# Optimization experiments

Hardware: AMD Instinct MI355X
Metric: run time of the kernel (lower is better)

## Reference

```python
import jax, jax.numpy as jnp
import numpy as np

B_, L, DM = 4, 1024, 1024
DI, DS, DR, DC = 1024, 16, 64, 4
NH = 4
DK = DM // NH


def setup_inputs() -> dict:
    key = jax.random.key(0)
    ks = jax.random.split(key, 16)
    def w(i, shape, scale=0.02):
        return jax.random.normal(ks[i], shape, dtype=jnp.float32) * scale
    inp = {
        "x": jax.random.normal(ks[0], (B_, L, DM), dtype=jnp.float32),
        "xx": jax.random.normal(ks[1], (B_, L, DI), dtype=jnp.float32),
        "in_proj_w": w(2, (DI, DM)),
        "conv_w": w(3, (DI, 1, DC)),            # depthwise conv, groups=DI
        "conv_b": jnp.zeros((DI,), jnp.float32),
        "x_proj_w": w(4, (DR + 2 * DS, DI)),
        "dt_proj_w": w(5, (DI, DR)),
        "dt_proj_b": jnp.zeros((DI,), jnp.float32),
        "A_log": jnp.log(jnp.tile(jnp.arange(1, DS + 1, dtype=jnp.float32)[None, :], (DI, 1))),
        "D": jnp.ones((DI,), jnp.float32),
        "wq": w(6, (DM, DM)), "bq": jnp.zeros((DM,), jnp.float32),
        "wk": w(7, (DM, DM)), "bk": jnp.zeros((DM,), jnp.float32),
        "wv": w(8, (DM, DM)), "bv": jnp.zeros((DM,), jnp.float32),
        "wo": w(9, (DM, DM)), "bo": jnp.zeros((DM,), jnp.float32),
    }
    return inp


def _stim_forward(x, xx, in_proj_w, conv_w, conv_b, x_proj_w, dt_proj_w, dt_proj_b,
                  A_log, D, wq, bq, wk, bk, wv, bv, wo, bo):
    b, l, _ = xx.shape
    # query branch: in_proj (Linear, no bias)
    q = x @ in_proj_w.T                                    # (b, l, DI)
    # kv branch: causal depthwise conv1d (padding d_conv-1, truncated to l)
    xc = jnp.transpose(xx, (0, 2, 1))                      # (b, DI, l)
    xc = jax.lax.conv_general_dilated(
        xc, conv_w, window_strides=(1,), padding=[(DC - 1, 0)],
        dimension_numbers=("NCH", "OIH", "NCH"), feature_group_count=DI)
    xc = xc + conv_b[None, :, None]
    u = jax.nn.silu(jnp.transpose(xc, (0, 2, 1)))          # (b, l, DI)
    # SSM parameter projections
    A = -jnp.exp(A_log)                                    # (DI, DS)
    x_dbl = u @ x_proj_w.T                                 # (b, l, DR+2*DS)
    delta, Bm, Cm = jnp.split(x_dbl, [DR, DR + DS], axis=-1)
    delta = jax.nn.softplus(delta @ dt_proj_w.T + dt_proj_b)  # (b, l, DI)
    deltaA = jnp.exp(jnp.einsum("bld,dn->bldn", delta, A))    # (b, l, DI, DS)
    deltaBu = jnp.einsum("bld,bln,bld->bldn", delta, Bm, u)   # (b, l, DI, DS)
    # selective scan over time
    def step(h, inp):
        dA_t, dBu_t, C_t = inp
        h = dA_t * h + dBu_t                               # (b, DI, DS)
        y_t = jnp.einsum("bdn,bn->bd", h, C_t)             # (b, DI)
        return h, y_t
    h0 = jnp.zeros((b, DI, DS), dtype=u.dtype)
    _, ys = jax.lax.scan(step, h0, (jnp.moveaxis(deltaA, 1, 0),
                                    jnp.moveaxis(deltaBu, 1, 0),
                                    jnp.moveaxis(Cm, 1, 0)))
    y = jnp.moveaxis(ys, 0, 1) + u * D                     # (b, l, DI)
    # cross attention: query = q, key/value = y
    Q = (q @ wq.T + bq).reshape(b, l, NH, DK).transpose(0, 2, 1, 3)
    K = (y @ wk.T + bk).reshape(b, l, NH, DK).transpose(0, 2, 1, 3)
    V = (y @ wv.T + bv).reshape(b, l, NH, DK).transpose(0, 2, 1, 3)
    scale = 1.0 / np.sqrt(DK).astype(np.float32)
    scores = jnp.einsum("bhqd,bhkd->bhqk", Q, K) * scale
    attn = jax.nn.softmax(scores, axis=-1)
    out = jnp.einsum("bhqk,bhkd->bhqd", attn, V)
    out = out.transpose(0, 2, 1, 3).reshape(b, l, DM)
    return out @ wo.T + bo


def reference(x, xx, in_proj_w, conv_w, conv_b, x_proj_w, dt_proj_w, dt_proj_b,
              A_log, D, wq, bq, wk, bk, wv, bv, wo, bo):
    return _stim_forward(x, xx, in_proj_w, conv_w, conv_b, x_proj_w, dt_proj_w,
                         dt_proj_b, A_log, D, wq, bq, wk, bk, wv, bv, wo, bo)
```

## Files before the change

### kernel.cpp

```cpp
#include <hip/hip_runtime.h>
#include <math.h>

#define B_  4
#define L_  1024
#define DM  1024
#define DI  1024
#define DS  16
#define DR  64
#define DCV 4
#define NH  4
#define DK  256

#define NCH 32
#define CHL (L_ / NCH)

typedef __attribute__((ext_vector_type(8))) short short8;
typedef __attribute__((ext_vector_type(4))) float floatx4;

static __device__ __forceinline__ unsigned short f2bf(float f) {
    unsigned int u = __float_as_uint(f);
    u += 0x7fffu + ((u >> 16) & 1u);
    return (unsigned short)(u >> 16);
}
static __device__ __forceinline__ float bf2f(unsigned short s) {
    return __uint_as_float(((unsigned int)s) << 16);
}

#define GLL(gp, lp) __builtin_amdgcn_global_load_lds( \
        (const __attribute__((address_space(1))) void*)(gp), \
        (__attribute__((address_space(3))) void*)(lp), 16, 0, 0)

static __device__ __forceinline__ void xcd_rect(int gx, int gy, int& tx, int& ty)
{
    int n = blockIdx.x + gx * blockIdx.y;
    if ((gx & 1) == 0 && (gy & 3) == 0) {
        int xcd = n & 7, j = n >> 3;
        int hx = gx >> 1, qy = gy >> 2;
        tx = (xcd & 1) * hx + (j % hx);
        ty = (xcd >> 1) * qy + (j / hx);
    } else {
        tx = blockIdx.x; ty = blockIdx.y;
    }
}

struct PrepArgs {
    const float* xx; const float* cw; const float* cb;
    float* u; unsigned short* ub;
    const float* xs; unsigned short* xd;
    const float* s[7]; unsigned short* d[7];
    int n[7];
    int ns[7];
};

__global__ __launch_bounds__(256) void prep(PrepArgs pa)
{
    int bid = blockIdx.x, tid = threadIdx.x;
    if (bid < 16384) {
        int idx = bid * 256 + tid;
        int d = idx & (DI - 1);
        int l = (idx >> 10) & (L_ - 1);
        int b = idx >> 20;
        const float* xb = pa.xx + (size_t)b * L_ * DI + d;
        float z = pa.cb[d];
#pragma unroll
        for (int j = 0; j < DCV; j++) {
            int t = l - (DCV - 1) + j;
            if (t >= 0) z += xb[(size_t)t * DI] * pa.cw[d * DCV + j];
        }
        float v = z / (1.0f + __expf(-z));
        pa.u[idx] = v;
        pa.ub[idx] = f2bf(v);
        return;
    }
    bid -= 16384;
    if (bid < 4096) {
        int i = (bid * 256 + tid) * 4;
        float4 v = *(const float4*)(pa.xs + i);
        ushort4 o;
        o.x = f2bf(v.x); o.y = f2bf(v.y); o.z = f2bf(v.z); o.w = f2bf(v.w);
        *(ushort4*)(pa.xd + i) = o;
        return;
    }
    bid -= 4096;
#pragma unroll
    for (int r = 0; r < 7; r++) {
        int nb = pa.n[r] >> 10;
        if (bid < nb) {
            int i = (bid * 256 + tid) * 4;
            int ns = pa.ns[r];
            const float* s = pa.s[r];
            ushort4 o;
            if (i + 4 <= ns) {
                float4 v = *(const float4*)(s + i);
                o.x = f2bf(v.x); o.y = f2bf(v.y); o.z = f2bf(v.z); o.w = f2bf(v.w);
            } else {
                float v[4];
#pragma unroll
                for (int j = 0; j < 4; j++) v[j] = (i + j < ns) ? s[i + j] : 0.f;
                o.x = f2bf(v[0]); o.y = f2bf(v[1]); o.z = f2bf(v[2]); o.w = f2bf(v[3]);
            }
            *(ushort4*)(pa.d[r] + i) = o;
            return;
        }
        bid -= nb;
    }
}

struct GDesc {
    const unsigned short* A;
    const unsigned short* W;
    const float* bias;
    float* Cf;
    unsigned short* Cb;
    int K, lda, ldw, ldc, ldc2;
    int mode;
    float scale;
    int gx, gy;
};
struct GArgs { GDesc g[3]; };

__global__ __launch_bounds__(256) void gemm_multi(GArgs ga)
{
    GDesc g = ga.g[blockIdx.z];
    int bx, by;
    xcd_rect(gridDim.x, gridDim.y, bx, by);
    if (bx >= g.gx || by >= g.gy) return;

    __shared__ __align__(16) unsigned short Asm[3][128 * 32];
    __shared__ __align__(16) unsigned short Bsm[3][128 * 32];

    int tid = threadIdx.x;
    int wid = tid >> 6;
    int lane = tid & 63;
    int wm = wid & 1, wn = wid >> 1;
    int lr = lane & 15, quad = lane >> 4;
    int sq = quad ^ ((lr >> 1) & 3);

    const unsigned short* Ab = g.A + (size_t)by * 128 * g.lda;
    const unsigned short* Wb = g.W + (size_t)bx * 128 * g.ldw;

    int srow = tid >> 2;
    int scol = ((tid & 3) ^ ((tid >> 3) & 3)) * 8;
    const unsigned short* Ap = Ab + (size_t)srow * g.lda + scol;
    const unsigned short* Wp = Wb + (size_t)srow * g.ldw + scol;

    int lbase = (wid * 16) * 32;

    floatx4 acc[4][4];
#pragma unroll
    for (int i = 0; i < 4; i++)
#pragma unroll
        for (int j = 0; j < 4; j++) acc[i][j] = (floatx4){0.f, 0.f, 0.f, 0.f};

#define STAGE_M(buf) do { \
        GLL(Ap, &Asm[buf][lbase]); \
        GLL(Ap + (size_t)64 * g.lda, &Asm[buf][lbase + 64 * 32]); \
        GLL(Wp, &Bsm[buf][lbase]); \
        GLL(Wp + (size_t)64 * g.ldw, &Bsm[buf][lbase + 64 * 32]); \
        Ap += 32; Wp += 32; \
    } while (0)

    int nK = g.K >> 5;
    STAGE_M(0);
    if (nK > 1) STAGE_M(1);

    int cur = 0, stg = 2;
    for (int k = 0; k < nK - 1; k++) {
        asm volatile("s_waitcnt vmcnt(4)" ::: "memory");
        __builtin_amdgcn_s_barrier();
        __builtin_amdgcn_sched_barrier(0);

        short8 af[4], bf[4];
#pragma unroll
        for (int mt = 0; mt < 4; mt++)
            af[mt] = *(const short8*)&Asm[cur][(wm * 64 + mt * 16 + lr) * 32 + sq * 8];
#pragma unroll
        for (int nt = 0; nt < 4; nt++)
            bf[nt] = *(const short8*)&Bsm[cur][(wn * 64 + nt * 16 + lr) * 32 + sq * 8];

        if (k + 2 < nK) {
            STAGE_M(stg);
            stg = (stg == 2) ? 0 : stg + 1;
        }

        __builtin_amdgcn_s_setprio(1);
#pragma unroll
        for (int mt = 0; mt < 4; mt++)
#pragma unroll
            for (int nt = 0; nt < 4; nt++)
                acc[mt][nt] = __builtin_amdgcn_mfma_f32_16x16x32_bf16(
                    af[mt], bf[nt], acc[mt][nt], 0, 0, 0);
        __builtin_amdgcn_s_setprio(0);
        cur = (cur == 2) ? 0 : cur + 1;
    }
    {
        asm volatile("s_waitcnt vmcnt(0)" ::: "memory");
        __builtin_amdgcn_s_barrier();
        __builtin_amdgcn_sched_barrier(0);

        short8 af[4], bf[4];
#pragma unroll
        for (int mt = 0; mt < 4; mt++)
            af[mt] = *(const short8*)&Asm[cur][(wm * 64 + mt * 16 + lr) * 32 + sq * 8];
#pragma unroll
        for (int nt = 0; nt < 4; nt++)
            bf[nt] = *(const short8*)&Bsm[cur][(wn * 64 + nt * 16 + lr) * 32 + sq * 8];
        __builtin_amdgcn_s_setprio(1);
#pragma unroll
        for (int mt = 0; mt < 4; mt++)
#pragma unroll
            for (int nt = 0; nt < 4; nt++)
                acc[mt][nt] = __builtin_amdgcn_mfma_f32_16x16x32_bf16(
                    af[mt], bf[nt], acc[mt][nt], 0, 0, 0);
        __builtin_amdgcn_s_setprio(0);
    }
#undef STAGE_M

    int bm = by * 128, bn = bx * 128;
    int m = g.mode & 3;
#pragma unroll
    for (int mt = 0; mt < 4; mt++) {
#pragma unroll
        for (int nt = 0; nt < 4; nt++) {
            int row0 = bm + wm * 64 + mt * 16 + quad * 4;
            int col = bn + wn * 64 + nt * 16 + lr;
            float bv = g.bias ? g.bias[col] : 0.f;
#pragma unroll
            for (int i = 0; i < 4; i++) {
                float v = acc[mt][nt][i] * g.scale + bv;
                if (g.mode & 4) v = (v > 15.f) ? v : log1pf(__expf(v));
                if (m == 0) {
                    g.Cf[(size_t)(row0 + i) * g.ldc + col] = v;
                } else if (m == 1) {
                    g.Cb[(size_t)(row0 + i) * g.ldc + col] = f2bf(v);
                } else {
                    g.Cf[(size_t)(row0 + i) * g.ldc + col] = v;
                    g.Cb[(size_t)(row0 + i) * g.ldc2 + col] = f2bf(v);
                }
            }
        }
    }
}

__global__ __launch_bounds__(256) void gemm_batched(
    const unsigned short* __restrict__ A, const unsigned short* __restrict__ W,
    unsigned short* __restrict__ C,
    int K, int lda, int ldw, int ldc,
    long long sA1, long long sA2, long long sW1, long long sW2,
    long long sC1, long long sC2, float scale)
{
    __shared__ __align__(16) unsigned short Asm[3][128 * 32];
    __shared__ __align__(16) unsigned short Bsm[3][128 * 32];

    int bx, by;
    xcd_rect(gridDim.x, gridDim.y, bx, by);

    int z = blockIdx.z;
    long long bq = z >> 2, hq = z & 3;
    int tid = threadIdx.x;
    int wid = tid >> 6;
    int lane = tid & 63;
    int wm = wid & 1, wn = wid >> 1;
    int lr = lane & 15, quad = lane >> 4;
    int sq = quad ^ ((lr >> 1) & 3);

    const unsigned short* Ab = A + bq * sA1 + hq * sA2 + (size_t)by * 128 * lda;
    const unsigned short* Wb = W + bq * sW1 + hq * sW2 + (size_t)bx * 128 * ldw;

    int srow = tid >> 2;
    int scol = ((tid & 3) ^ ((tid >> 3) & 3)) * 8;
    const unsigned short* Ap = Ab + (size_t)srow * lda + scol;
    const unsigned short* Wp = Wb + (size_t)srow * ldw + scol;

    int lbase = (wid * 16) * 32;

    floatx4 acc[4][4];
#pragma unroll
    for (int i = 0; i < 4; i++)
#pragma unroll
        for (int j = 0; j < 4; j++) acc[i][j] = (floatx4){0.f, 0.f, 0.f, 0.f};

#define STAGE_B(buf) do { \
        GLL(Ap, &Asm[buf][lbase]); \
        GLL(Ap + (size_t)64 * lda, &Asm[buf][lbase + 64 * 32]); \
        GLL(Wp, &Bsm[buf][lbase]); \
        GLL(Wp + (size_t)64 * ldw, &Bsm[buf][lbase + 64 * 32]); \
        Ap += 32; Wp += 32; \
    } while (0)

    int nK = K >> 5;
    STAGE_B(0);
    if (nK > 1) STAGE_B(1);

    int cur = 0, stg = 2;
    for (int k = 0; k < nK - 1; k++) {
        asm volatile("s_waitcnt vmcnt(4)" ::: "memory");
        __builtin_amdgcn_s_barrier();
        __builtin_amdgcn_sched_barrier(0);

        short8 af[4], bf[4];
#pragma unroll
        for (int mt = 0; mt < 4; mt++)
            af[mt] = *(const short8*)&Asm[cur][(wm * 64 + mt * 16 + lr) * 32 + sq * 8];
#pragma unroll
        for (int nt = 0; nt < 4; nt++)
            bf[nt] = *(const short8*)&Bsm[cur][(wn * 64 + nt * 16 + lr) * 32 + sq * 8];

        if (k + 2 < nK) {
            STAGE_B(stg);
            stg = (stg == 2) ? 0 : stg + 1;
        }

        __builtin_amdgcn_s_setprio(1);
#pragma unroll
        for (int mt = 0; mt < 4; mt++)
#pragma unroll
            for (int nt = 0; nt < 4; nt++)
                acc[mt][nt] = __builtin_amdgcn_mfma_f32_16x16x32_bf16(
                    af[mt], bf[nt], acc[mt][nt], 0, 0, 0);
        __builtin_amdgcn_s_setprio(0);
        cur = (cur == 2) ? 0 : cur + 1;
    }
    {
        asm volatile("s_waitcnt vmcnt(0)" ::: "memory");
        __builtin_amdgcn_s_barrier();
        __builtin_amdgcn_sched_barrier(0);

        short8 af[4], bf[4];
#pragma unroll
        for (int mt = 0; mt < 4; mt++)
            af[mt] = *(const short8*)&Asm[cur][(wm * 64 + mt * 16 + lr) * 32 + sq * 8];
#pragma unroll
        for (int nt = 0; nt < 4; nt++)
            bf[nt] = *(const short8*)&Bsm[cur][(wn * 64 + nt * 16 + lr) * 32 + sq * 8];
        __builtin_amdgcn_s_setprio(1);
#pragma unroll
        for (int mt = 0; mt < 4; mt++)
#pragma unroll
            for (int nt = 0; nt < 4; nt++)
                acc[mt][nt] = __builtin_amdgcn_mfma_f32_16x16x32_bf16(
                    af[mt], bf[nt], acc[mt][nt], 0, 0, 0);
        __builtin_amdgcn_s_setprio(0);
    }
#undef STAGE_B

    long long coff = bq * sC1 + hq * sC2;
    int bm = by * 128, bn = bx * 128;
    unsigned short* Cb = C + coff;

#pragma unroll
    for (int mt = 0; mt < 4; mt++) {
#pragma unroll
        for (int nt = 0; nt < 4; nt++) {
            int row0 = bm + wm * 64 + mt * 16 + quad * 4;
            int col = bn + wn * 64 + nt * 16 + lr;
#pragma unroll
            for (int i = 0; i < 4; i++)
                Cb[(size_t)(row0 + i) * ldc + col] = f2bf(acc[mt][nt][i] * scale);
        }
    }
}

__global__ __launch_bounds__(256) void scan_a(
    const float* __restrict__ delta, const float* __restrict__ u,
    const float* __restrict__ xdbl, const float* __restrict__ A_log,
    float* __restrict__ Hc, float* __restrict__ sumdv)
{
    int gid = blockIdx.x * 256 + threadIdx.x;
    int c = gid >> 12;
    int bd = gid & 4095;
    int b = bd >> 10, d = bd & 1023;

    float a[16];
#pragma unroll
    for (int j = 0; j < 4; j++) {
        float4 al = *(const float4*)(A_log + d * 16 + j * 4);
        a[j * 4 + 0] = -__expf(al.x); a[j * 4 + 1] = -__expf(al.y);
        a[j * 4 + 2] = -__expf(al.z); a[j * 4 + 3] = -__expf(al.w);
    }
    float h[16];
#pragma unroll
    for (int n = 0; n < 16; n++) h[n] = 0.f;
    float sd = 0.f;

    int t0 = c * CHL;
    const float* dp = delta + ((size_t)(b * L_) + t0) * DI + d;
    const float* up = u + ((size_t)(b * L_) + t0) * DI + d;
    const float* xp = xdbl + ((size_t)(b * L_) + t0) * 128;

#pragma unroll 4
    for (int t = 0; t < CHL; t++) {
        float dv = dp[t * DI];
        float uv = up[t * DI];
        float duv = dv * uv;
        sd += dv;
        float Bv[16];
#pragma unroll
        for (int j = 0; j < 4; j++) {
            float4 bq = *(const float4*)(xp + t * 128 + 64 + j * 4);
            Bv[j * 4 + 0] = bq.x; Bv[j * 4 + 1] = bq.y;
            Bv[j * 4 + 2] = bq.z; Bv[j * 4 + 3] = bq.w;
        }
#pragma unroll
        for (int n = 0; n < 16; n++)
            h[n] = __expf(dv * a[n]) * h[n] + duv * Bv[n];
    }

    float* hp = Hc + ((size_t)c * 4096 + bd) * 16;
#pragma unroll
    for (int j = 0; j < 4; j++)
        *(float4*)(hp + j * 4) = make_float4(h[j * 4], h[j * 4 + 1], h[j * 4 + 2], h[j * 4 + 3]);
    sumdv[c * 4096 + bd] = sd;
}

__global__ __launch_bounds__(256) void scan_b(
    float* __restrict__ Hc, const float* __restrict__ sumdv,
    const float* __restrict__ A_log)
{
    int bd = blockIdx.x * 256 + threadIdx.x;
    int d = bd & 1023;

    float a[16];
#pragma unroll
    for (int j = 0; j < 4; j++) {
        float4 al = *(const float4*)(A_log + d * 16 + j * 4);
        a[j * 4 + 0] = -__expf(al.x); a[j * 4 + 1] = -__expf(al.y);
        a[j * 4 + 2] = -__expf(al.z); a[j * 4 + 3] = -__expf(al.w);
    }
    float H[16];
#pragma unroll
    for (int n = 0; n < 16; n++) H[n] = 0.f;

    for (int c = 0; c < NCH; c++) {
        float* hp = Hc + ((size_t)c * 4096 + bd) * 16;
        float sdv = sumdv[c * 4096 + bd];
        float hc[16];
#pragma unroll
        for (int j = 0; j < 4; j++) {
            float4 q = *(const float4*)(hp + j * 4);
            hc[j * 4 + 0] = q.x; hc[j * 4 + 1] = q.y; hc[j * 4 + 2] = q.z; hc[j * 4 + 3] = q.w;
        }
#pragma unroll
        for (int j = 0; j < 4; j++)
            *(float4*)(hp + j * 4) = make_float4(H[j * 4], H[j * 4 + 1], H[j * 4 + 2], H[j * 4 + 3]);
#pragma unroll
        for (int n = 0; n < 16; n++)
            H[n] = __expf(a[n] * sdv) * H[n] + hc[n];
    }
}

__global__ __launch_bounds__(256) void scan_c(
    const float* __restrict__ delta, const float* __restrict__ u,
    const float* __restrict__ xdbl, const float* __restrict__ A_log,
    const float* __restrict__ Dv, const float* __restrict__ Hstart,
    unsigned short* __restrict__ y)
{
    int gid = blockIdx.x * 256 + threadIdx.x;
    int c = gid >> 12;
    int bd = gid & 4095;
    int b = bd >> 10, d = bd & 1023;

    float a[16];
#pragma unroll
    for (int j = 0; j < 4; j++) {
        float4 al = *(const float4*)(A_log + d * 16 + j * 4);
        a[j * 4 + 0] = -__expf(al.x); a[j * 4 + 1] = -__expf(al.y);
        a[j * 4 + 2] = -__expf(al.z); a[j * 4 + 3] = -__expf(al.w);
    }
    float h[16];
    const float* hp = Hstart + ((size_t)c * 4096 + bd) * 16;
#pragma unroll
    for (int j = 0; j < 4; j++) {
        float4 q = *(const float4*)(hp + j * 4);
        h[j * 4 + 0] = q.x; h[j * 4 + 1] = q.y; h[j * 4 + 2] = q.z; h[j * 4 + 3] = q.w;
    }
    float Dd = Dv[d];

    int t0 = c * CHL;
    const float* dp = delta + ((size_t)(b * L_) + t0) * DI + d;
    const float* up = u + ((size_t)(b * L_) + t0) * DI + d;
    const float* xp = xdbl + ((size_t)(b * L_) + t0) * 128;
    unsigned short* yp = y + ((size_t)(b * L_) + t0) * DI + d;

#pragma unroll 4
    for (int t = 0; t < CHL; t++) {
        float dv = dp[t * DI];
        float uv = up[t * DI];
        float duv = dv * uv;
        float Bv[16], Cv[16];
#pragma unroll
        for (int j = 0; j < 4; j++) {
            float4 bq = *(const float4*)(xp + t * 128 + 64 + j * 4);
            Bv[j * 4 + 0] = bq.x; Bv[j * 4 + 1] = bq.y;
            Bv[j * 4 + 2] = bq.z; Bv[j * 4 + 3] = bq.w;
            float4 cq = *(const float4*)(xp + t * 128 + 80 + j * 4);
            Cv[j * 4 + 0] = cq.x; Cv[j * 4 + 1] = cq.y;
            Cv[j * 4 + 2] = cq.z; Cv[j * 4 + 3] = cq.w;
        }
        float ys = 0.f;
#pragma unroll
        for (int n = 0; n < 16; n++) {
            h[n] = __expf(dv * a[n]) * h[n] + duv * Bv[n];
            ys += h[n] * Cv[n];
        }
        yp[t * DI] = f2bf(ys + uv * Dd);
    }
}

__global__ __launch_bounds__(256) void softmax_transpose(
    unsigned short* __restrict__ S,
    const unsigned short* __restrict__ V, unsigned short* __restrict__ VT)
{
    __shared__ unsigned short tl[32][36];
    int bid = blockIdx.x;
    if (bid < 4096) {
        int row = bid * 4 + (threadIdx.x >> 6);
        int lane = threadIdx.x & 63;
        unsigned short* p = S + (size_t)row * 1024;

        float v[16];
#pragma unroll
        for (int ch = 0; ch < 4; ch++) {
            ushort4 u4 = *(const ushort4*)(p + ch * 256 + lane * 4);
            v[ch * 4 + 0] = bf2f(u4.x); v[ch * 4 + 1] = bf2f(u4.y);
            v[ch * 4 + 2] = bf2f(u4.z); v[ch * 4 + 3] = bf2f(u4.w);
        }
        float m = -1e30f;
#pragma unroll
        for (int i = 0; i < 16; i++) m = fmaxf(m, v[i]);
#pragma unroll
        for (int off = 32; off >= 1; off >>= 1) m = fmaxf(m, __shfl_xor(m, off));
        float s = 0.f;
#pragma unroll
        for (int i = 0; i < 16; i++) { v[i] = __expf(v[i] - m); s += v[i]; }
#pragma unroll
        for (int off = 32; off >= 1; off >>= 1) s += __shfl_xor(s, off);
        float inv = 1.0f / s;
#pragma unroll
        for (int ch = 0; ch < 4; ch++) {
            ushort4 o;
            o.x = f2bf(v[ch * 4 + 0] * inv); o.y = f2bf(v[ch * 4 + 1] * inv);
            o.z = f2bf(v[ch * 4 + 2] * inv); o.w = f2bf(v[ch * 4 + 3] * inv);
            *(ushort4*)(p + ch * 256 + lane * 4) = o;
        }
        return;
    }
    int tb = bid - 4096;
    int bh = tb >> 8;
    int rem = tb & 255;
    int d0 = (rem >> 5) * 32;
    int l0 = (rem & 31) * 32;
    int b = bh >> 2, h = bh & 3;
    int tid = threadIdx.x;
    int r = tid >> 3, c4 = (tid & 7) * 4;

    const unsigned short* src = V + ((size_t)(b * L_ + l0 + r)) * 1024 + h * DK + d0 + c4;
    ushort4 v = *(const ushort4*)src;
    tl[r][c4 + 0] = v.x; tl[r][c4 + 1] = v.y; tl[r][c4 + 2] = v.z; tl[r][c4 + 3] = v.w;
    __syncthreads();

    unsigned short* dst = VT + ((size_t)bh * DK + d0 + r) * L_ + l0 + c4;
    ushort4 o;
    o.x = tl[c4 + 0][r]; o.y = tl[c4 + 1][r]; o.z = tl[c4 + 2][r]; o.w = tl[c4 + 3][r];
    *(ushort4*)dst = o;
}

extern "C" void kernel_launch(void* const* d_in, const int* in_sizes, int n_in,
                              void* d_out, int out_size, void* d_ws, size_t ws_size,
                              hipStream_t stream)
{
    const float* x         = (const float*)d_in[0];
    const float* xx        = (const float*)d_in[1];
    const float* in_proj_w = (const float*)d_in[2];
    const float* conv_w    = (const float*)d_in[3];
    const float* conv_b    = (const float*)d_in[4];
    const float* x_proj_w  = (const float*)d_in[5];
    const float* dt_proj_w = (const float*)d_in[6];
    const float* dt_proj_b = (const float*)d_in[7];
    const float* A_log     = (const float*)d_in[8];
    const float* Dvec      = (const float*)d_in[9];
    const float* wq        = (const float*)d_in[10];
    const float* bq        = (const float*)d_in[11];
    const float* wk        = (const float*)d_in[12];
    const float* bk        = (const float*)d_in[13];
    const float* wv        = (const float*)d_in[14];
    const float* bv        = (const float*)d_in[15];
    const float* wo        = (const float*)d_in[16];
    const float* bo        = (const float*)d_in[17];
    float* out = (float*)d_out;

    char* w = (char*)d_ws;
    const size_t MB = 1024 * 1024, KB = 1024;
    float*          u_f    = (float*)(w + 0);
    float*          delta  = (float*)(w + 16 * MB);
    unsigned short* Sbuf   = (unsigned short*)(w + 0);
    unsigned short* x_bf   = (unsigned short*)(w + 32 * MB);
    unsigned short* Q_bf   = x_bf;
    unsigned short* q_bf   = (unsigned short*)(w + 40 * MB);
    unsigned short* VT     = q_bf;
    unsigned short* y_bf   = (unsigned short*)(w + 48 * MB);
    unsigned short* AO     = y_bf;
    unsigned short* K_bf   = (unsigned short*)(w + 56 * MB);
    unsigned short* V_bf   = (unsigned short*)(w + 64 * MB);
    unsigned short* u_bf   = (unsigned short*)(w + 72 * MB);
    float*          Hc     = (float*)(w + 72 * MB);
    float*          xdbl   = (float*)(w + 80 * MB);
    unsigned short* xdblb  = (unsigned short*)(w + 82 * MB);
    unsigned short* w_in   = (unsigned short*)(w + 83 * MB);
    unsigned short* w_q    = (unsigned short*)(w + 85 * MB);
    unsigned short* w_k    = (unsigned short*)(w + 87 * MB);
    unsigned short* w_v    = (unsigned short*)(w + 89 * MB);
    unsigned short* w_o    = (unsigned short*)(w + 91 * MB);
    unsigned short* w_xp   = (unsigned short*)(w + 93 * MB);
    unsigned short* w_dt   = (unsigned short*)(w + 93 * MB + 256 * KB);
    float*          sumdv  = (float*)(w + 93 * MB + 384 * KB);

    dim3 blk(256);
    const long long LL = L_;

    PrepArgs pa;
    pa.xx = xx; pa.cw = conv_w; pa.cb = conv_b; pa.u = u_f; pa.ub = u_bf;
    pa.xs = x; pa.xd = x_bf;
    pa.s[0] = in_proj_w; pa.d[0] = w_in; pa.n[0] = 1048576; pa.ns[0] = 1048576;
    pa.s[1] = wq;        pa.d[1] = w_q;  pa.n[1] = 1048576; pa.ns[1] = 1048576;
    pa.s[2] = wk;        pa.d[2] = w_k;  pa.n[2] = 1048576; pa.ns[2] = 1048576;
    pa.s[3] = wv;        pa.d[3] = w_v;  pa.n[3] = 1048576; pa.ns[3] = 1048576;
    pa.s[4] = wo;        pa.d[4] = w_o;  pa.n[4] = 1048576; pa.ns[4] = 1048576;
    pa.s[5] = x_proj_w;  pa.d[5] = w_xp; pa.n[5] = 131072;  pa.ns[5] = 98304;
    pa.s[6] = dt_proj_w; pa.d[6] = w_dt; pa.n[6] = 65536;   pa.ns[6] = 65536;
    prep<<<dim3(25792), blk, 0, stream>>>(pa);

    {
        GArgs ga = {};
        ga.g[0] = (GDesc){x_bf, w_in, nullptr, nullptr, q_bf,
                          1024, 1024, 1024, 1024, 0, 1, 1.0f, 8, 32};
        ga.g[1] = (GDesc){u_bf, w_xp, nullptr, xdbl, xdblb,
                          1024, 1024, 1024, 128, 128, 2, 1.0f, 1, 32};
        gemm_multi<<<dim3(8, 32, 2), blk, 0, stream>>>(ga);
    }
    {
        GArgs ga = {};
        ga.g[0] = (GDesc){xdblb, w_dt, dt_proj_b, delta, nullptr,
                          64, 128, 64, 1024, 0, 0 | 4, 1.0f, 8, 32};
        gemm_multi<<<dim3(8, 32, 1), blk, 0, stream>>>(ga);
    }
    scan_a<<<dim3(512), blk, 0, stream>>>(delta, u_f, xdbl, A_log, Hc, sumdv);
    scan_b<<<dim3(16), blk, 0, stream>>>(Hc, sumdv, A_log);
    scan_c<<<dim3(512), blk, 0, stream>>>(delta, u_f, xdbl, A_log, Dvec, Hc, y_bf);

    {
        GArgs ga = {};
        ga.g[0] = (GDesc){q_bf, w_q, bq, nullptr, Q_bf, 1024, 1024, 1024, 1024, 0, 1, 1.0f, 8, 32};
        ga.g[1] = (GDesc){y_bf, w_k, bk, nullptr, K_bf, 1024, 1024, 1024, 1024, 0, 1, 1.0f, 8, 32};
        ga.g[2] = (GDesc){y_bf, w_v, bv, nullptr, V_bf, 1024, 1024, 1024, 1024, 0, 1, 1.0f, 8, 32};
        gemm_multi<<<dim3(8, 32, 3), blk, 0, stream>>>(ga);
    }
    gemm_batched<<<dim3(8, 8, 16), blk, 0, stream>>>(Q_bf, K_bf, Sbuf,
        DK, 1024, 1024, 1024,
        LL * 1024, 256, LL * 1024, 256,
        4 * LL * 1024, LL * 1024, 0.0625f);
    softmax_transpose<<<dim3(8192), blk, 0, stream>>>(Sbuf, V_bf, VT);
    gemm_batched<<<dim3(2, 8, 16), blk, 0, stream>>>(Sbuf, VT, AO,
        1024, 1024, 1024, 1024,
        4 * LL * 1024, LL * 1024,
        4 * (long long)DK * 1024, (long long)DK * 1024,
        LL * 1024, 256, 1.0f);
    {
        GArgs ga = {};
        ga.g[0] = (GDesc){AO, w_o, bo, out, nullptr, 1024, 1024, 1024, 1024, 0, 0, 1.0f, 8, 32};
        gemm_multi<<<dim3(8, 32, 1), blk, 0, stream>>>(ga);
    }
}
```

Before: 398.4 us.

## Pre-pack weights into MFMA fragment layout and load B directly to registers

```diff
diff --git a/kernel.cpp b/kernel.cpp
--- a/kernel.cpp
+++ b/kernel.cpp
@@ -49,7 +49,9 @@
     const float* xs; unsigned short* xd;
     const float* s[7]; unsigned short* d[7];
     int n[7];
-    int ns[7];
+    int kk[7];
+    int rn[7];
+    int nts[7];
 };
 
 __global__ __launch_bounds__(256) void prep(PrepArgs pa)
@@ -84,22 +86,30 @@
     bid -= 4096;
 #pragma unroll
     for (int r = 0; r < 7; r++) {
-        int nb = pa.n[r] >> 10;
+        int nb = pa.n[r] >> 11;
         if (bid < nb) {
-            int i = (bid * 256 + tid) * 4;
-            int ns = pa.ns[r];
-            const float* s = pa.s[r];
-            ushort4 o;
-            if (i + 4 <= ns) {
-                float4 v = *(const float4*)(s + i);
-                o.x = f2bf(v.x); o.y = f2bf(v.y); o.z = f2bf(v.z); o.w = f2bf(v.w);
+            int c = bid * 256 + tid;
+            int t = c & 63;
+            int blk = c >> 6;
+            int nt16 = blk & ((1 << pa.nts[r]) - 1);
+            int kc = blk >> pa.nts[r];
+            int K = pa.kk[r];
+            int nrow = nt16 * 16 + (t & 15);
+            int k = kc * 32 + (t >> 4) * 8;
+            ushort4 o0, o1;
+            if (nrow < pa.rn[r]) {
+                const float* s = pa.s[r] + (size_t)nrow * K + k;
+                float4 v0 = *(const float4*)(s);
+                float4 v1 = *(const float4*)(s + 4);
+                o0.x = f2bf(v0.x); o0.y = f2bf(v0.y); o0.z = f2bf(v0.z); o0.w = f2bf(v0.w);
+                o1.x = f2bf(v1.x); o1.y = f2bf(v1.y); o1.z = f2bf(v1.z); o1.w = f2bf(v1.w);
             } else {
-                float v[4];
-#pragma unroll
-                for (int j = 0; j < 4; j++) v[j] = (i + j < ns) ? s[i + j] : 0.f;
-                o.x = f2bf(v[0]); o.y = f2bf(v[1]); o.z = f2bf(v[2]); o.w = f2bf(v[3]);
+                o0.x = o0.y = o0.z = o0.w = 0;
+                o1.x = o1.y = o1.z = o1.w = 0;
             }
-            *(ushort4*)(pa.d[r] + i) = o;
+            unsigned short* dp = pa.d[r] + (size_t)c * 8;
+            *(ushort4*)(dp) = o0;
+            *(ushort4*)(dp + 4) = o1;
             return;
         }
         bid -= nb;
@@ -127,7 +137,6 @@
     if (bx >= g.gx || by >= g.gy) return;
 
     __shared__ __align__(16) unsigned short Asm[3][128 * 32];
-    __shared__ __align__(16) unsigned short Bsm[3][128 * 32];
 
     int tid = threadIdx.x;
     int wid = tid >> 6;
@@ -137,12 +146,13 @@
     int sq = quad ^ ((lr >> 1) & 3);
 
     const unsigned short* Ab = g.A + (size_t)by * 128 * g.lda;
-    const unsigned short* Wb = g.W + (size_t)bx * 128 * g.ldw;
-
     int srow = tid >> 2;
     int scol = ((tid & 3) ^ ((tid >> 3) & 3)) * 8;
     const unsigned short* Ap = Ab + (size_t)srow * g.lda + scol;
-    const unsigned short* Wp = Wb + (size_t)srow * g.ldw + scol;
+
+    int nTiles = g.ldw >> 4;
+    size_t kcStride = (size_t)nTiles << 9;
+    const unsigned short* Wf = g.W + ((size_t)(bx * 8 + wn * 4) * 64 + lane) * 8;
 
     int lbase = (wid * 16) * 32;
 
@@ -155,66 +165,71 @@
 #define STAGE_M(buf) do { \
         GLL(Ap, &Asm[buf][lbase]); \
         GLL(Ap + (size_t)64 * g.lda, &Asm[buf][lbase + 64 * 32]); \
-        GLL(Wp, &Bsm[buf][lbase]); \
-        GLL(Wp + (size_t)64 * g.ldw, &Bsm[buf][lbase + 64 * 32]); \
-        Ap += 32; Wp += 32; \
+        Ap += 32; \
     } while (0)
+#define LOADB(dst, kc) do { \
+        const unsigned short* wp_ = Wf + (size_t)(kc) * kcStride; \
+        dst[0] = *(const short8*)(wp_); \
+        dst[1] = *(const short8*)(wp_ + 512); \
+        dst[2] = *(const short8*)(wp_ + 1024); \
+        dst[3] = *(const short8*)(wp_ + 1536); \
+    } while (0)
 
     int nK = g.K >> 5;
+    short8 bfE[4], bfO[4];
     STAGE_M(0);
     if (nK > 1) STAGE_M(1);
+    __builtin_amdgcn_sched_barrier(0);
+    LOADB(bfE, 0);
 
     int cur = 0, stg = 2;
-    for (int k = 0; k < nK - 1; k++) {
-        asm volatile("s_waitcnt vmcnt(4)" ::: "memory");
+    for (int k = 0; k < nK; k += 2) {
+        asm volatile("s_waitcnt vmcnt(6)" ::: "memory");
         __builtin_amdgcn_s_barrier();
         __builtin_amdgcn_sched_barrier(0);
-
-        short8 af[4], bf[4];
+        short8 af[4];
 #pragma unroll
         for (int mt = 0; mt < 4; mt++)
             af[mt] = *(const short8*)&Asm[cur][(wm * 64 + mt * 16 + lr) * 32 + sq * 8];
-#pragma unroll
-        for (int nt = 0; nt < 4; nt++)
-            bf[nt] = *(const short8*)&Bsm[cur][(wn * 64 + nt * 16 + lr) * 32 + sq * 8];
-
-        if (k + 2 < nK) {
-            STAGE_M(stg);
-            stg = (stg == 2) ? 0 : stg + 1;
-        }
-
+        if (k + 2 < nK) { STAGE_M(stg); stg = (stg == 2) ? 0 : stg + 1; }
+        __builtin_amdgcn_sched_barrier(0);
+        if (k + 1 < nK) LOADB(bfO, k + 1);
+        __builtin_amdgcn_sched_barrier(0);
         __builtin_amdgcn_s_setprio(1);
 #pragma unroll
         for (int mt = 0; mt < 4; mt++)
 #pragma unroll
             for (int nt = 0; nt < 4; nt++)
                 acc[mt][nt] = __builtin_amdgcn_mfma_f32_16x16x32_bf16(
-                    af[mt], bf[nt], acc[mt][nt], 0, 0, 0);
+                    af[mt], bfE[nt], acc[mt][nt], 0, 0, 0);
         __builtin_amdgcn_s_setprio(0);
         cur = (cur == 2) ? 0 : cur + 1;
-    }
-    {
-        asm volatile("s_waitcnt vmcnt(0)" ::: "memory");
-        __builtin_amdgcn_s_barrier();
-        __builtin_amdgcn_sched_barrier(0);
-
-        short8 af[4], bf[4];
-#pragma unroll
-        for (int mt = 0; mt < 4; mt++)
-            af[mt] = *(const short8*)&Asm[cur][(wm * 64 + mt * 16 + lr) * 32 + sq * 8];
-#pragma unroll
-        for (int nt = 0; nt < 4; nt++)
-            bf[nt] = *(const short8*)&Bsm[cur][(wn * 64 + nt * 16 + lr) * 32 + sq * 8];
-        __builtin_amdgcn_s_setprio(1);
-#pragma unroll
-        for (int mt = 0; mt < 4; mt++)
-#pragma unroll
-            for (int nt = 0; nt < 4; nt++)
-                acc[mt][nt] = __builtin_amdgcn_mfma_f32_16x16x32_bf16(
-                    af[mt], bf[nt], acc[mt][nt], 0, 0, 0);
-        __builtin_amdgcn_s_setprio(0);
+
+        if (k + 1 < nK) {
+            asm volatile("s_waitcnt vmcnt(6)" ::: "memory");
+            __builtin_amdgcn_s_barrier();
+            __builtin_amdgcn_sched_barrier(0);
+            short8 af2[4];
+#pragma unroll
+            for (int mt = 0; mt < 4; mt++)
+                af2[mt] = *(const short8*)&Asm[cur][(wm * 64 + mt * 16 + lr) * 32 + sq * 8];
+            if (k + 3 < nK) { STAGE_M(stg); stg = (stg == 2) ? 0 : stg + 1; }
+            __builtin_amdgcn_sched_barrier(0);
+            if (k + 2 < nK) LOADB(bfE, k + 2);
+            __builtin_amdgcn_sched_barrier(0);
+            __builtin_amdgcn_s_setprio(1);
+#pragma unroll
+            for (int mt = 0; mt < 4; mt++)
+#pragma unroll
+                for (int nt = 0; nt < 4; nt++)
+                    acc[mt][nt] = __builtin_amdgcn_mfma_f32_16x16x32_bf16(
+                        af2[mt], bfO[nt], acc[mt][nt], 0, 0, 0);
+            __builtin_amdgcn_s_setprio(0);
+            cur = (cur == 2) ? 0 : cur + 1;
+        }
     }
 #undef STAGE_M
+#undef LOADB
 
     int bm = by * 128, bn = bx * 128;
     int m = g.mode & 3;
@@ -621,27 +636,27 @@
     PrepArgs pa;
     pa.xx = xx; pa.cw = conv_w; pa.cb = conv_b; pa.u = u_f; pa.ub = u_bf;
     pa.xs = x; pa.xd = x_bf;
-    pa.s[0] = in_proj_w; pa.d[0] = w_in; pa.n[0] = 1048576; pa.ns[0] = 1048576;
-    pa.s[1] = wq;        pa.d[1] = w_q;  pa.n[1] = 1048576; pa.ns[1] = 1048576;
-    pa.s[2] = wk;        pa.d[2] = w_k;  pa.n[2] = 1048576; pa.ns[2] = 1048576;
-    pa.s[3] = wv;        pa.d[3] = w_v;  pa.n[3] = 1048576; pa.ns[3] = 1048576;
-    pa.s[4] = wo;        pa.d[4] = w_o;  pa.n[4] = 1048576; pa.ns[4] = 1048576;
-    pa.s[5] = x_proj_w;  pa.d[5] = w_xp; pa.n[5] = 131072;  pa.ns[5] = 98304;
-    pa.s[6] = dt_proj_w; pa.d[6] = w_dt; pa.n[6] = 65536;   pa.ns[6] = 65536;
-    prep<<<dim3(25792), blk, 0, stream>>>(pa);
+    pa.s[0] = in_proj_w; pa.d[0] = w_in; pa.n[0] = 1048576; pa.kk[0] = 1024; pa.rn[0] = 1024; pa.nts[0] = 6;
+    pa.s[1] = wq;        pa.d[1] = w_q;  pa.n[1] = 1048576; pa.kk[1] = 1024; pa.rn[1] = 1024; pa.nts[1] = 6;
+    pa.s[2] = wk;        pa.d[2] = w_k;  pa.n[2] = 1048576; pa.kk[2] = 1024; pa.rn[2] = 1024; pa.nts[2] = 6;
+    pa.s[3] = wv;        pa.d[3] = w_v;  pa.n[3] = 1048576; pa.kk[3] = 1024; pa.rn[3] = 1024; pa.nts[3] = 6;
+    pa.s[4] = wo;        pa.d[4] = w_o;  pa.n[4] = 1048576; pa.kk[4] = 1024; pa.rn[4] = 1024; pa.nts[4] = 6;
+    pa.s[5] = x_proj_w;  pa.d[5] = w_xp; pa.n[5] = 131072;  pa.kk[5] = 1024; pa.rn[5] = 96;   pa.nts[5] = 3;
+    pa.s[6] = dt_proj_w; pa.d[6] = w_dt; pa.n[6] = 65536;   pa.kk[6] = 64;   pa.rn[6] = 1024; pa.nts[6] = 6;
+    prep<<<dim3(23136), blk, 0, stream>>>(pa);
 
     {
         GArgs ga = {};
         ga.g[0] = (GDesc){x_bf, w_in, nullptr, nullptr, q_bf,
                           1024, 1024, 1024, 1024, 0, 1, 1.0f, 8, 32};
         ga.g[1] = (GDesc){u_bf, w_xp, nullptr, xdbl, xdblb,
-                          1024, 1024, 1024, 128, 128, 2, 1.0f, 1, 32};
+                          1024, 1024, 128, 128, 128, 2, 1.0f, 1, 32};
         gemm_multi<<<dim3(8, 32, 2), blk, 0, stream>>>(ga);
     }
     {
         GArgs ga = {};
         ga.g[0] = (GDesc){xdblb, w_dt, dt_proj_b, delta, nullptr,
-                          64, 128, 64, 1024, 0, 0 | 4, 1.0f, 8, 32};
+                          64, 128, 1024, 1024, 0, 0 | 4, 1.0f, 8, 32};
         gemm_multi<<<dim3(8, 32, 1), blk, 0, stream>>>(ga);
     }
     scan_a<<<dim3(512), blk, 0, stream>>>(delta, u_f, xdbl, A_log, Hc, sumdv);
```

New measurement: 424.2 us. 6.5% more time.

## Add 256x256-tile 512-thread GEMM kernel for the square 1024x1024 projections

Applied to the files above, without the earlier changes.

```diff
diff --git a/kernel.cpp b/kernel.cpp
--- a/kernel.cpp
+++ b/kernel.cpp
@@ -237,6 +237,133 @@
                     g.Cf[(size_t)(row0 + i) * g.ldc + col] = v;
                     g.Cb[(size_t)(row0 + i) * g.ldc2 + col] = f2bf(v);
                 }
+            }
+        }
+    }
+}
+
+struct BDesc {
+    const unsigned short* A;
+    const unsigned short* W;
+    const float* bias;
+    float* Cf;
+    unsigned short* Cb;
+    int mode;
+};
+struct BArgs { BDesc g[3]; };
+
+__global__ __launch_bounds__(512, 2) void gemm_big(BArgs ga)
+{
+    BDesc g = ga.g[blockIdx.z];
+    int bx, by;
+    xcd_rect(gridDim.x, gridDim.y, bx, by);
+
+    __shared__ __align__(16) unsigned short Asm[3][256 * 32];
+    __shared__ __align__(16) unsigned short Bsm[3][256 * 32];
+
+    int tid = threadIdx.x;
+    int wid = tid >> 6;
+    int lane = tid & 63;
+    int wm = wid & 1, wn = wid >> 1;
+    int lr = lane & 15, quad = lane >> 4;
+    int sq = quad ^ ((lr >> 1) & 3);
+
+    const unsigned short* Ab = g.A + (size_t)by * 256 * 1024;
+    const unsigned short* Wb = g.W + (size_t)bx * 256 * 1024;
+
+    int srow = tid >> 2;
+    int scol = ((tid & 3) ^ ((tid >> 3) & 3)) * 8;
+    const unsigned short* Ap = Ab + (size_t)srow * 1024 + scol;
+    const unsigned short* Wp = Wb + (size_t)srow * 1024 + scol;
+
+    int lb1 = (wid * 16) * 32;
+    int lb2 = (128 + wid * 16) * 32;
+
+    floatx4 acc[8][4];
+#pragma unroll
+    for (int i = 0; i < 8; i++)
+#pragma unroll
+        for (int j = 0; j < 4; j++) acc[i][j] = (floatx4){0.f, 0.f, 0.f, 0.f};
+
+#define STAGE_G(buf) do { \
+        GLL(Ap, &Asm[buf][lb1]); \
+        GLL(Ap + (size_t)128 * 1024, &Asm[buf][lb2]); \
+        GLL(Wp, &Bsm[buf][lb1]); \
+        GLL(Wp + (size_t)128 * 1024, &Bsm[buf][lb2]); \
+        Ap += 32; Wp += 32; \
+    } while (0)
+
+    const int nK = 32;
+    STAGE_G(0);
+    STAGE_G(1);
+
+    int cur = 0, stg = 2;
+    for (int k = 0; k < nK - 1; k++) {
+        asm volatile("s_waitcnt vmcnt(4)" ::: "memory");
+        __builtin_amdgcn_s_barrier();
+        __builtin_amdgcn_sched_barrier(0);
+
+        short8 af[8], bf[4];
+#pragma unroll
+        for (int mt = 0; mt < 8; mt++)
+            af[mt] = *(const short8*)&Asm[cur][(wm * 128 + mt * 16 + lr) * 32 + sq * 8];
+#pragma unroll
+        for (int nt = 0; nt < 4; nt++)
+            bf[nt] = *(const short8*)&Bsm[cur][(wn * 64 + nt * 16 + lr) * 32 + sq * 8];
+
+        if (k + 2 < nK) {
+            STAGE_G(stg);
+            stg = (stg == 2) ? 0 : stg + 1;
+        }
+
+        __builtin_amdgcn_s_setprio(1);
+#pragma unroll
+        for (int mt = 0; mt < 8; mt++)
+#pragma unroll
+            for (int nt = 0; nt < 4; nt++)
+                acc[mt][nt] = __builtin_amdgcn_mfma_f32_16x16x32_bf16(
+                    af[mt], bf[nt], acc[mt][nt], 0, 0, 0);
+        __builtin_amdgcn_s_setprio(0);
+        cur = (cur == 2) ? 0 : cur + 1;
+    }
+    {
+        asm volatile("s_waitcnt vmcnt(0)" ::: "memory");
+        __builtin_amdgcn_s_barrier();
+        __builtin_amdgcn_sched_barrier(0);
+
+        short8 af[8], bf[4];
+#pragma unroll
+        for (int mt = 0; mt < 8; mt++)
+            af[mt] = *(const short8*)&Asm[cur][(wm * 128 + mt * 16 + lr) * 32 + sq * 8];
+#pragma unroll
+        for (int nt = 0; nt < 4; nt++)
+            bf[nt] = *(const short8*)&Bsm[cur][(wn * 64 + nt * 16 + lr) * 32 + sq * 8];
+        __builtin_amdgcn_s_setprio(1);
+#pragma unroll
+        for (int mt = 0; mt < 8; mt++)
+#pragma unroll
+            for (int nt = 0; nt < 4; nt++)
+                acc[mt][nt] = __builtin_amdgcn_mfma_f32_16x16x32_bf16(
+                    af[mt], bf[nt], acc[mt][nt], 0, 0, 0);
+        __builtin_amdgcn_s_setprio(0);
+    }
+#undef STAGE_G
+
+    int bm = by * 256, bn = bx * 256;
+#pragma unroll
+    for (int mt = 0; mt < 8; mt++) {
+#pragma unroll
+        for (int nt = 0; nt < 4; nt++) {
+            int row0 = bm + wm * 128 + mt * 16 + quad * 4;
+            int col = bn + wn * 64 + nt * 16 + lr;
+            float bv = g.bias ? g.bias[col] : 0.f;
+#pragma unroll
+            for (int i = 0; i < 4; i++) {
+                float v = acc[mt][nt][i] + bv;
+                if (g.mode == 0)
+                    g.Cf[(size_t)(row0 + i) * 1024 + col] = v;
+                else
+                    g.Cb[(size_t)(row0 + i) * 1024 + col] = f2bf(v);
             }
         }
     }
@@ -632,11 +759,14 @@
 
     {
         GArgs ga = {};
-        ga.g[0] = (GDesc){x_bf, w_in, nullptr, nullptr, q_bf,
-                          1024, 1024, 1024, 1024, 0, 1, 1.0f, 8, 32};
-        ga.g[1] = (GDesc){u_bf, w_xp, nullptr, xdbl, xdblb,
+        ga.g[0] = (GDesc){u_bf, w_xp, nullptr, xdbl, xdblb,
                           1024, 1024, 1024, 128, 128, 2, 1.0f, 1, 32};
-        gemm_multi<<<dim3(8, 32, 2), blk, 0, stream>>>(ga);
+        gemm_multi<<<dim3(1, 32, 1), blk, 0, stream>>>(ga);
+    }
+    {
+        BArgs ba = {};
+        ba.g[0] = (BDesc){x_bf, w_in, nullptr, nullptr, q_bf, 1};
+        gemm_big<<<dim3(4, 16, 1), dim3(512), 0, stream>>>(ba);
     }
     {
         GArgs ga = {};
@@ -649,11 +779,11 @@
     scan_c<<<dim3(512), blk, 0, stream>>>(delta, u_f, xdbl, A_log, Dvec, Hc, y_bf);
 
     {
-        GArgs ga = {};
-        ga.g[0] = (GDesc){q_bf, w_q, bq, nullptr, Q_bf, 1024, 1024, 1024, 1024, 0, 1, 1.0f, 8, 32};
-        ga.g[1] = (GDesc){y_bf, w_k, bk, nullptr, K_bf, 1024, 1024, 1024, 1024, 0, 1, 1.0f, 8, 32};
-        ga.g[2] = (GDesc){y_bf, w_v, bv, nullptr, V_bf, 1024, 1024, 1024, 1024, 0, 1, 1.0f, 8, 32};
-        gemm_multi<<<dim3(8, 32, 3), blk, 0, stream>>>(ga);
+        BArgs ba = {};
+        ba.g[0] = (BDesc){q_bf, w_q, bq, nullptr, Q_bf, 1};
+        ba.g[1] = (BDesc){y_bf, w_k, bk, nullptr, K_bf, 1};
+        ba.g[2] = (BDesc){y_bf, w_v, bv, nullptr, V_bf, 1};
+        gemm_big<<<dim3(4, 16, 3), dim3(512), 0, stream>>>(ba);
     }
     gemm_batched<<<dim3(8, 8, 16), blk, 0, stream>>>(Q_bf, K_bf, Sbuf,
         DK, 1024, 1024, 1024,
@@ -666,8 +796,8 @@
         4 * (long long)DK * 1024, (long long)DK * 1024,
         LL * 1024, 256, 1.0f);
     {
-        GArgs ga = {};
-        ga.g[0] = (GDesc){AO, w_o, bo, out, nullptr, 1024, 1024, 1024, 1024, 0, 0, 1.0f, 8, 32};
-        gemm_multi<<<dim3(8, 32, 1), blk, 0, stream>>>(ga);
-    }
-}
+        BArgs ba = {};
+        ba.g[0] = (BDesc){AO, w_o, bo, out, nullptr, 0};
+        gemm_big<<<dim3(4, 16, 1), dim3(512), 0, stream>>>(ba);
+    }
+}
```

Measured after the change: 435.1 us. 1.09x slower.
